# Optimization experiments

Hardware: AMD Instinct MI355X
Metric: run time of the kernel (lower is better)

The kernel has to match this reference:

```python
import jax, jax.numpy as jnp
import numpy as np

S, B, N, K, D, H = 4, 8, 2048, 16, 32, 128


def setup_inputs() -> dict:
    key = jax.random.key(0)
    ks = jax.random.split(key, 7)
    x = jax.random.normal(ks[0], (S, B, N, D), dtype=jnp.float32)
    mu = jax.random.normal(ks[1], (S, B, K, D), dtype=jnp.float32)
    tau = jax.random.uniform(ks[2], (S, B, K, D), dtype=jnp.float32)  # precisions > 0
    # Linear(3D -> H); stored as (3D, H) i.e. transpose of torch's (H, 3D) weight
    W1 = jax.random.normal(ks[3], (3 * D, H), dtype=jnp.float32) * (1.0 / np.sqrt(3 * D))
    b1 = jax.random.normal(ks[4], (H,), dtype=jnp.float32) * 0.01
    W2 = jax.random.normal(ks[5], (H, 1), dtype=jnp.float32) * (1.0 / np.sqrt(H))
    b2 = jax.random.normal(ks[6], (1,), dtype=jnp.float32) * 0.01
    return {"x": x, "mu": mu, "tau": tau, "W1": W1, "b1": b1, "W2": W2, "b2": b2}


def reference(x, mu, tau, W1, b1, W2, b2):
    # Original torch code materializes var = cat([x_expand, mu_expand, tau_expand], -1)
    # of shape (S,B,N,K,3D) then applies Linear(3D,H). Mathematically identical:
    # split W1 rows into the x / mu / tau blocks and add the partial projections,
    # which avoids building the (S,B,N,K,3D) concat tensor.
    d = x.shape[-1]
    Wx, Wm, Wt = W1[:d], W1[d:2 * d], W1[2 * d:]
    hx = jnp.einsum('sbnd,dh->sbnh', x, Wx)                       # (S,B,N,H)
    hk = jnp.einsum('sbkd,dh->sbkh', mu, Wm) \
       + jnp.einsum('sbkd,dh->sbkh', tau, Wt)                     # (S,B,K,H)
    h = jnp.tanh(hx[:, :, :, None, :] + hk[:, :, None, :, :] + b1)  # (S,B,N,K,H)
    gamma = jnp.einsum('sbnkh,h->sbnk', h, W2[:, 0]) + b2[0]        # (S,B,N,K)
    q_probs = jax.nn.softmax(gamma, axis=-1)
    return q_probs
```

## Files before the change

kernel.cpp:

```cpp
#include <hip/hip_runtime.h>
#include <math.h>

typedef _Float16 half_t;
typedef __attribute__((ext_vector_type(8))) _Float16 half8;

#define EXP2F(x) __builtin_amdgcn_exp2f(x)
#define RCPF(x)  __builtin_amdgcn_rcpf(x)
#define C_SCALE 2.8853900817779268f

__global__ __launch_bounds__(256, 4) void fused_kernel(
    const float* __restrict__ x, const float* __restrict__ mu,
    const float* __restrict__ tau, const float* __restrict__ W1,
    const float* __restrict__ b1, const float* __restrict__ W2,
    float* __restrict__ out) {
  __shared__ __align__(16) float  sX[64][36];
  __shared__ __align__(16) half_t sEx[64][136];
  __shared__ __align__(16) half_t sEk[16][136];
  __shared__ __align__(16) half_t sW2[128];

  int t = threadIdx.x;
  int row0 = blockIdx.x * 64;
  int sb = row0 >> 11;

  const float4* x4 = (const float4*)(x + (size_t)row0 * 32);
#pragma unroll
  for (int i = 0; i < 2; ++i) {
    int j = i * 256 + t;
    int n = j >> 3, d4 = j & 7;
    float4 v = x4[j];
    v.x *= C_SCALE; v.y *= C_SCALE; v.z *= C_SCALE; v.w *= C_SCALE;
    *(float4*)&sX[n][d4 * 4] = v;
  }
  if (t < 16) {
    float4 a = ((const float4*)W2)[2 * t];
    float4 b = ((const float4*)W2)[2 * t + 1];
    half8 hv;
    hv[0] = (half_t)(-2.f * a.x); hv[1] = (half_t)(-2.f * a.y);
    hv[2] = (half_t)(-2.f * a.z); hv[3] = (half_t)(-2.f * a.w);
    hv[4] = (half_t)(-2.f * b.x); hv[5] = (half_t)(-2.f * b.y);
    hv[6] = (half_t)(-2.f * b.z); hv[7] = (half_t)(-2.f * b.w);
    *(half8*)&sW2[t * 8] = hv;
  }
  __syncthreads();

  {
    int hg = t & 15, rg = t >> 4;
    int h0 = hg * 8, r0 = rg * 4;
    float acc[4][8];
#pragma unroll
    for (int j = 0; j < 4; ++j)
#pragma unroll
      for (int l = 0; l < 8; ++l) acc[j][l] = 0.f;
    const float* Wp = W1 + h0;
#pragma unroll 4
    for (int d = 0; d < 32; ++d) {
      float4 wa = *(const float4*)(Wp + d * 128);
      float4 wb = *(const float4*)(Wp + d * 128 + 4);
      float w[8] = {wa.x, wa.y, wa.z, wa.w, wb.x, wb.y, wb.z, wb.w};
#pragma unroll
      for (int j = 0; j < 4; ++j) {
        float xv = sX[r0 + j][d];
#pragma unroll
        for (int l = 0; l < 8; ++l) acc[j][l] = fmaf(xv, w[l], acc[j][l]);
      }
    }
#pragma unroll
    for (int j = 0; j < 4; ++j) {
      half8 hv;
#pragma unroll
      for (int l = 0; l < 8; ++l) hv[l] = (half_t)EXP2F(acc[j][l]);
      *(half8*)&sEx[r0 + j][h0] = hv;
    }
  }

  {
    int k = t >> 4, h0 = (t & 15) * 8;
    const float4* mu4  = (const float4*)(mu  + ((size_t)sb * 16 + k) * 32);
    const float4* tau4 = (const float4*)(tau + ((size_t)sb * 16 + k) * 32);
    float acc[8];
    {
      float4 ba = *(const float4*)(b1 + h0);
      float4 bb = *(const float4*)(b1 + h0 + 4);
      acc[0] = ba.x; acc[1] = ba.y; acc[2] = ba.z; acc[3] = ba.w;
      acc[4] = bb.x; acc[5] = bb.y; acc[6] = bb.z; acc[7] = bb.w;
    }
    const float* Wm = W1 + 32 * 128 + h0;
    const float* Wt = W1 + 64 * 128 + h0;
#pragma unroll 2
    for (int d4 = 0; d4 < 8; ++d4) {
      float4 m4 = mu4[d4], t4 = tau4[d4];
      float mv4[4] = {m4.x, m4.y, m4.z, m4.w};
      float tv4[4] = {t4.x, t4.y, t4.z, t4.w};
#pragma unroll
      for (int dd = 0; dd < 4; ++dd) {
        int d = d4 * 4 + dd;
        float4 wma = *(const float4*)(Wm + d * 128);
        float4 wmb = *(const float4*)(Wm + d * 128 + 4);
        float4 wta = *(const float4*)(Wt + d * 128);
        float4 wtb = *(const float4*)(Wt + d * 128 + 4);
        float wm[8] = {wma.x, wma.y, wma.z, wma.w, wmb.x, wmb.y, wmb.z, wmb.w};
        float wt[8] = {wta.x, wta.y, wta.z, wta.w, wtb.x, wtb.y, wtb.z, wtb.w};
        float mv = mv4[dd], tv = tv4[dd];
#pragma unroll
        for (int l = 0; l < 8; ++l) {
          acc[l] = fmaf(mv, wm[l], acc[l]);
          acc[l] = fmaf(tv, wt[l], acc[l]);
        }
      }
    }
    half8 hv;
#pragma unroll
    for (int l = 0; l < 8; ++l) hv[l] = (half_t)EXP2F(C_SCALE * acc[l]);
    *(half8*)&sEk[k][h0] = hv;
  }
  __syncthreads();

  int kg = t & 7, rg = t >> 3;
  int r0 = rg * 2, k0 = kg * 2;
  float a00 = 0.f, a01 = 0.f, a10 = 0.f, a11 = 0.f;
#pragma unroll 2
  for (int h8 = 0; h8 < 16; ++h8) {
    half8 ex0 = *(const half8*)&sEx[r0][h8 * 8];
    half8 ex1 = *(const half8*)&sEx[r0 + 1][h8 * 8];
    half8 ekv0 = *(const half8*)&sEk[k0][h8 * 8];
    half8 ekv1 = *(const half8*)&sEk[k0 + 1][h8 * 8];
    half8 wv = *(const half8*)&sW2[h8 * 8];
#pragma unroll
    for (int j = 0; j < 8; ++j) {
      float e0 = (float)ex0[j], e1 = (float)ex1[j];
      float f0 = (float)ekv0[j], f1 = (float)ekv1[j];
      float w = (float)wv[j];
      a00 = fmaf(w, RCPF(fmaf(e0, f0, 1.0f)), a00);
      a01 = fmaf(w, RCPF(fmaf(e0, f1, 1.0f)), a01);
      a10 = fmaf(w, RCPF(fmaf(e1, f0, 1.0f)), a10);
      a11 = fmaf(w, RCPF(fmaf(e1, f1, 1.0f)), a11);
    }
  }

  const float l2e = 1.4426950408889634f;
  {
    float m = fmaxf(a00, a01);
#pragma unroll
    for (int s = 1; s < 8; s <<= 1) m = fmaxf(m, __shfl_xor(m, s, 8));
    float p0 = EXP2F((a00 - m) * l2e), p1 = EXP2F((a01 - m) * l2e);
    float sum = p0 + p1;
#pragma unroll
    for (int s = 1; s < 8; s <<= 1) sum += __shfl_xor(sum, s, 8);
    float inv = RCPF(sum);
    float2 o = make_float2(p0 * inv, p1 * inv);
    *(float2*)&out[(size_t)(row0 + r0) * 16 + k0] = o;
  }
  {
    float m = fmaxf(a10, a11);
#pragma unroll
    for (int s = 1; s < 8; s <<= 1) m = fmaxf(m, __shfl_xor(m, s, 8));
    float p0 = EXP2F((a10 - m) * l2e), p1 = EXP2F((a11 - m) * l2e);
    float sum = p0 + p1;
#pragma unroll
    for (int s = 1; s < 8; s <<= 1) sum += __shfl_xor(sum, s, 8);
    float inv = RCPF(sum);
    float2 o = make_float2(p0 * inv, p1 * inv);
    *(float2*)&out[(size_t)(row0 + r0 + 1) * 16 + k0] = o;
  }
}

extern "C" void kernel_launch(void* const* d_in, const int* in_sizes, int n_in,
                              void* d_out, int out_size, void* d_ws, size_t ws_size,
                              hipStream_t stream) {
  const float* x   = (const float*)d_in[0];
  const float* mu  = (const float*)d_in[1];
  const float* tau = (const float*)d_in[2];
  const float* W1  = (const float*)d_in[3];
  const float* b1  = (const float*)d_in[4];
  const float* W2  = (const float*)d_in[5];
  float* out = (float*)d_out;
  (void)in_sizes; (void)n_in; (void)out_size; (void)d_ws; (void)ws_size;

  fused_kernel<<<1024, 256, 0, stream>>>(x, mu, tau, W1, b1, W2, out);
}
```

Before: 103.9 us.

## Stage W1 x-block in padded LDS, alias it for Ex, keep Ek/W2 fp32

The x-projection weights (first 32 rows of W1) are now loaded cooperatively into a padded shared buffer, so the per-row projection reads shared memory instead of issuing repeated global float4 loads. That buffer is then reused, after an extra barrier, to hold the fp16 exp(x) tile, and the x projection moves after the mu/tau projection. The Ek and W2 tiles are kept in fp32 rather than fp16, which removes conversions in the inner loop but doubles their LDS reads. The cost is an extra __syncthreads and higher register pressure, since the exp(x) values are held in registers across a barrier.

```diff
diff --git a/kernel.cpp b/kernel.cpp
--- a/kernel.cpp
+++ b/kernel.cpp
@@ -13,10 +13,10 @@
     const float* __restrict__ tau, const float* __restrict__ W1,
     const float* __restrict__ b1, const float* __restrict__ W2,
     float* __restrict__ out) {
-  __shared__ __align__(16) float  sX[64][36];
-  __shared__ __align__(16) half_t sEx[64][136];
-  __shared__ __align__(16) half_t sEk[16][136];
-  __shared__ __align__(16) half_t sW2[128];
+  __shared__ __align__(16) float sX[64][36];
+  __shared__ __align__(16) unsigned char sU[32 * 560];
+  __shared__ __align__(16) float sEk[16][132];
+  __shared__ __align__(16) float sW2[128];
 
   int t = threadIdx.x;
   int row0 = blockIdx.x * 64;
@@ -31,47 +31,13 @@
     v.x *= C_SCALE; v.y *= C_SCALE; v.z *= C_SCALE; v.w *= C_SCALE;
     *(float4*)&sX[n][d4 * 4] = v;
   }
-  if (t < 16) {
-    float4 a = ((const float4*)W2)[2 * t];
-    float4 b = ((const float4*)W2)[2 * t + 1];
-    half8 hv;
-    hv[0] = (half_t)(-2.f * a.x); hv[1] = (half_t)(-2.f * a.y);
-    hv[2] = (half_t)(-2.f * a.z); hv[3] = (half_t)(-2.f * a.w);
-    hv[4] = (half_t)(-2.f * b.x); hv[5] = (half_t)(-2.f * b.y);
-    hv[6] = (half_t)(-2.f * b.z); hv[7] = (half_t)(-2.f * b.w);
-    *(half8*)&sW2[t * 8] = hv;
+#pragma unroll
+  for (int i = 0; i < 4; ++i) {
+    int j = i * 256 + t;
+    int d = j >> 5, f = j & 31;
+    *(float4*)(sU + d * 560 + f * 16 + (f >> 3) * 16) = ((const float4*)W1)[j];
   }
-  __syncthreads();
-
-  {
-    int hg = t & 15, rg = t >> 4;
-    int h0 = hg * 8, r0 = rg * 4;
-    float acc[4][8];
-#pragma unroll
-    for (int j = 0; j < 4; ++j)
-#pragma unroll
-      for (int l = 0; l < 8; ++l) acc[j][l] = 0.f;
-    const float* Wp = W1 + h0;
-#pragma unroll 4
-    for (int d = 0; d < 32; ++d) {
-      float4 wa = *(const float4*)(Wp + d * 128);
-      float4 wb = *(const float4*)(Wp + d * 128 + 4);
-      float w[8] = {wa.x, wa.y, wa.z, wa.w, wb.x, wb.y, wb.z, wb.w};
-#pragma unroll
-      for (int j = 0; j < 4; ++j) {
-        float xv = sX[r0 + j][d];
-#pragma unroll
-        for (int l = 0; l < 8; ++l) acc[j][l] = fmaf(xv, w[l], acc[j][l]);
-      }
-    }
-#pragma unroll
-    for (int j = 0; j < 4; ++j) {
-      half8 hv;
-#pragma unroll
-      for (int l = 0; l < 8; ++l) hv[l] = (half_t)EXP2F(acc[j][l]);
-      *(half8*)&sEx[r0 + j][h0] = hv;
-    }
-  }
+  if (t < 128) sW2[t] = -2.0f * W2[t];
 
   {
     int k = t >> 4, h0 = (t & 15) * 8;
@@ -108,32 +74,74 @@
         }
       }
     }
-    half8 hv;
-#pragma unroll
-    for (int l = 0; l < 8; ++l) hv[l] = (half_t)EXP2F(C_SCALE * acc[l]);
-    *(half8*)&sEk[k][h0] = hv;
+    float4 e0, e1;
+    e0.x = EXP2F(C_SCALE * acc[0]); e0.y = EXP2F(C_SCALE * acc[1]);
+    e0.z = EXP2F(C_SCALE * acc[2]); e0.w = EXP2F(C_SCALE * acc[3]);
+    e1.x = EXP2F(C_SCALE * acc[4]); e1.y = EXP2F(C_SCALE * acc[5]);
+    e1.z = EXP2F(C_SCALE * acc[6]); e1.w = EXP2F(C_SCALE * acc[7]);
+    *(float4*)&sEk[k][h0] = e0;
+    *(float4*)&sEk[k][h0 + 4] = e1;
   }
   __syncthreads();
 
-  int kg = t & 7, rg = t >> 3;
-  int r0 = rg * 2, k0 = kg * 2;
+  int hg = t & 15, rg = t >> 4;
+  int h0 = hg * 8, r0 = rg * 4;
+  half8 hv[4];
+  {
+    const unsigned char* wbase = sU + hg * 32 + (hg >> 2) * 16;
+    float acc[4][8];
+#pragma unroll
+    for (int j = 0; j < 4; ++j)
+#pragma unroll
+      for (int l = 0; l < 8; ++l) acc[j][l] = 0.f;
+#pragma unroll 4
+    for (int d = 0; d < 32; ++d) {
+      float4 wa = *(const float4*)(wbase + d * 560);
+      float4 wb = *(const float4*)(wbase + d * 560 + 16);
+      float w[8] = {wa.x, wa.y, wa.z, wa.w, wb.x, wb.y, wb.z, wb.w};
+#pragma unroll
+      for (int j = 0; j < 4; ++j) {
+        float xv = sX[r0 + j][d];
+#pragma unroll
+        for (int l = 0; l < 8; ++l) acc[j][l] = fmaf(xv, w[l], acc[j][l]);
+      }
+    }
+#pragma unroll
+    for (int j = 0; j < 4; ++j)
+#pragma unroll
+      for (int l = 0; l < 8; ++l) hv[j][l] = (half_t)EXP2F(acc[j][l]);
+  }
+  __syncthreads();
+
+  half_t (*sEx)[136] = (half_t(*)[136])sU;
+#pragma unroll
+  for (int j = 0; j < 4; ++j) *(half8*)&sEx[r0 + j][h0] = hv[j];
+  __syncthreads();
+
+  int kg = t & 7, rg2 = t >> 3;
+  int rp = rg2 * 2, k0 = kg * 2;
   float a00 = 0.f, a01 = 0.f, a10 = 0.f, a11 = 0.f;
 #pragma unroll 2
   for (int h8 = 0; h8 < 16; ++h8) {
-    half8 ex0 = *(const half8*)&sEx[r0][h8 * 8];
-    half8 ex1 = *(const half8*)&sEx[r0 + 1][h8 * 8];
-    half8 ekv0 = *(const half8*)&sEk[k0][h8 * 8];
-    half8 ekv1 = *(const half8*)&sEk[k0 + 1][h8 * 8];
-    half8 wv = *(const half8*)&sW2[h8 * 8];
+    half8 ex0 = *(const half8*)&sEx[rp][h8 * 8];
+    half8 ex1 = *(const half8*)&sEx[rp + 1][h8 * 8];
+    float4 f0a = *(const float4*)&sEk[k0][h8 * 8];
+    float4 f0b = *(const float4*)&sEk[k0][h8 * 8 + 4];
+    float4 f1a = *(const float4*)&sEk[k0 + 1][h8 * 8];
+    float4 f1b = *(const float4*)&sEk[k0 + 1][h8 * 8 + 4];
+    float4 wva = *(const float4*)&sW2[h8 * 8];
+    float4 wvb = *(const float4*)&sW2[h8 * 8 + 4];
+    float f0[8] = {f0a.x, f0a.y, f0a.z, f0a.w, f0b.x, f0b.y, f0b.z, f0b.w};
+    float f1[8] = {f1a.x, f1a.y, f1a.z, f1a.w, f1b.x, f1b.y, f1b.z, f1b.w};
+    float wv[8] = {wva.x, wva.y, wva.z, wva.w, wvb.x, wvb.y, wvb.z, wvb.w};
 #pragma unroll
     for (int j = 0; j < 8; ++j) {
       float e0 = (float)ex0[j], e1 = (float)ex1[j];
-      float f0 = (float)ekv0[j], f1 = (float)ekv1[j];
-      float w = (float)wv[j];
-      a00 = fmaf(w, RCPF(fmaf(e0, f0, 1.0f)), a00);
-      a01 = fmaf(w, RCPF(fmaf(e0, f1, 1.0f)), a01);
-      a10 = fmaf(w, RCPF(fmaf(e1, f0, 1.0f)), a10);
-      a11 = fmaf(w, RCPF(fmaf(e1, f1, 1.0f)), a11);
+      float w = wv[j];
+      a00 = fmaf(w, RCPF(fmaf(e0, f0[j], 1.0f)), a00);
+      a01 = fmaf(w, RCPF(fmaf(e0, f1[j], 1.0f)), a01);
+      a10 = fmaf(w, RCPF(fmaf(e1, f0[j], 1.0f)), a10);
+      a11 = fmaf(w, RCPF(fmaf(e1, f1[j], 1.0f)), a11);
     }
   }
 
@@ -148,7 +156,7 @@
     for (int s = 1; s < 8; s <<= 1) sum += __shfl_xor(sum, s, 8);
     float inv = RCPF(sum);
     float2 o = make_float2(p0 * inv, p1 * inv);
-    *(float2*)&out[(size_t)(row0 + r0) * 16 + k0] = o;
+    *(float2*)&out[(size_t)(row0 + rp) * 16 + k0] = o;
   }
   {
     float m = fmaxf(a10, a11);
@@ -160,7 +168,7 @@
     for (int s = 1; s < 8; s <<= 1) sum += __shfl_xor(sum, s, 8);
     float inv = RCPF(sum);
     float2 o = make_float2(p0 * inv, p1 * inv);
-    *(float2*)&out[(size_t)(row0 + r0 + 1) * 16 + k0] = o;
+    *(float2*)&out[(size_t)(row0 + rp + 1) * 16 + k0] = o;
   }
 }
 
```

Measured after the change: 98.68 us. 1.05x faster.

## Stage Wx in LDS, double block size, and alias sEx onto the weight buffer

Applied to the files above, without the earlier changes.

Each block now processes 128 rows with 512 threads, and the first 32 rows of W1 (Wx) are staged into a padded LDS buffer instead of being read from global memory inside the x-projection loop. That buffer is reused as sEx after an extra barrier, and the mu/tau projection is spread over 512 threads. The aim is to cut repeated global or L2 reads of W1 and to halve per-block setup across fewer, larger blocks. In exchange there are extra __syncthreads, more LDS per block, and only 512 blocks, which may lower occupancy.

```diff
diff --git a/kernel.cpp b/kernel.cpp
--- a/kernel.cpp
+++ b/kernel.cpp
@@ -3,33 +3,40 @@
 
 typedef _Float16 half_t;
 typedef __attribute__((ext_vector_type(8))) _Float16 half8;
+typedef __attribute__((ext_vector_type(4))) _Float16 half4;
 
 #define EXP2F(x) __builtin_amdgcn_exp2f(x)
 #define RCPF(x)  __builtin_amdgcn_rcpf(x)
 #define C_SCALE 2.8853900817779268f
 
-__global__ __launch_bounds__(256, 4) void fused_kernel(
+__global__ __launch_bounds__(512, 4) void fused_kernel(
     const float* __restrict__ x, const float* __restrict__ mu,
     const float* __restrict__ tau, const float* __restrict__ W1,
     const float* __restrict__ b1, const float* __restrict__ W2,
     float* __restrict__ out) {
-  __shared__ __align__(16) float  sX[64][36];
-  __shared__ __align__(16) half_t sEx[64][136];
+  __shared__ __align__(16) float sX[128][36];
+  __shared__ __align__(16) unsigned char sU[128 * 272];
   __shared__ __align__(16) half_t sEk[16][136];
   __shared__ __align__(16) half_t sW2[128];
 
   int t = threadIdx.x;
-  int row0 = blockIdx.x * 64;
+  int row0 = blockIdx.x * 128;
   int sb = row0 >> 11;
 
   const float4* x4 = (const float4*)(x + (size_t)row0 * 32);
 #pragma unroll
   for (int i = 0; i < 2; ++i) {
-    int j = i * 256 + t;
+    int j = i * 512 + t;
     int n = j >> 3, d4 = j & 7;
     float4 v = x4[j];
     v.x *= C_SCALE; v.y *= C_SCALE; v.z *= C_SCALE; v.w *= C_SCALE;
     *(float4*)&sX[n][d4 * 4] = v;
+  }
+#pragma unroll
+  for (int i = 0; i < 2; ++i) {
+    int j = i * 512 + t;
+    int d = j >> 5, f = j & 31;
+    *(float4*)(sU + d * 560 + f * 16 + (f >> 3) * 16) = ((const float4*)W1)[j];
   }
   if (t < 16) {
     float4 a = ((const float4*)W2)[2 * t];
@@ -41,48 +48,15 @@
     hv[6] = (half_t)(-2.f * b.z); hv[7] = (half_t)(-2.f * b.w);
     *(half8*)&sW2[t * 8] = hv;
   }
-  __syncthreads();
 
   {
-    int hg = t & 15, rg = t >> 4;
-    int h0 = hg * 8, r0 = rg * 4;
-    float acc[4][8];
-#pragma unroll
-    for (int j = 0; j < 4; ++j)
-#pragma unroll
-      for (int l = 0; l < 8; ++l) acc[j][l] = 0.f;
-    const float* Wp = W1 + h0;
-#pragma unroll 4
-    for (int d = 0; d < 32; ++d) {
-      float4 wa = *(const float4*)(Wp + d * 128);
-      float4 wb = *(const float4*)(Wp + d * 128 + 4);
-      float w[8] = {wa.x, wa.y, wa.z, wa.w, wb.x, wb.y, wb.z, wb.w};
-#pragma unroll
-      for (int j = 0; j < 4; ++j) {
-        float xv = sX[r0 + j][d];
-#pragma unroll
-        for (int l = 0; l < 8; ++l) acc[j][l] = fmaf(xv, w[l], acc[j][l]);
-      }
-    }
-#pragma unroll
-    for (int j = 0; j < 4; ++j) {
-      half8 hv;
-#pragma unroll
-      for (int l = 0; l < 8; ++l) hv[l] = (half_t)EXP2F(acc[j][l]);
-      *(half8*)&sEx[r0 + j][h0] = hv;
-    }
-  }
-
-  {
-    int k = t >> 4, h0 = (t & 15) * 8;
+    int k = t >> 5, h0 = (t & 31) * 4;
     const float4* mu4  = (const float4*)(mu  + ((size_t)sb * 16 + k) * 32);
     const float4* tau4 = (const float4*)(tau + ((size_t)sb * 16 + k) * 32);
-    float acc[8];
+    float acc[4];
     {
       float4 ba = *(const float4*)(b1 + h0);
-      float4 bb = *(const float4*)(b1 + h0 + 4);
       acc[0] = ba.x; acc[1] = ba.y; acc[2] = ba.z; acc[3] = ba.w;
-      acc[4] = bb.x; acc[5] = bb.y; acc[6] = bb.z; acc[7] = bb.w;
     }
     const float* Wm = W1 + 32 * 128 + h0;
     const float* Wt = W1 + 64 * 128 + h0;
@@ -94,42 +68,78 @@
 #pragma unroll
       for (int dd = 0; dd < 4; ++dd) {
         int d = d4 * 4 + dd;
-        float4 wma = *(const float4*)(Wm + d * 128);
-        float4 wmb = *(const float4*)(Wm + d * 128 + 4);
-        float4 wta = *(const float4*)(Wt + d * 128);
-        float4 wtb = *(const float4*)(Wt + d * 128 + 4);
-        float wm[8] = {wma.x, wma.y, wma.z, wma.w, wmb.x, wmb.y, wmb.z, wmb.w};
-        float wt[8] = {wta.x, wta.y, wta.z, wta.w, wtb.x, wtb.y, wtb.z, wtb.w};
+        float4 wm = *(const float4*)(Wm + d * 128);
+        float4 wt = *(const float4*)(Wt + d * 128);
+        float wmv[4] = {wm.x, wm.y, wm.z, wm.w};
+        float wtv[4] = {wt.x, wt.y, wt.z, wt.w};
         float mv = mv4[dd], tv = tv4[dd];
 #pragma unroll
-        for (int l = 0; l < 8; ++l) {
-          acc[l] = fmaf(mv, wm[l], acc[l]);
-          acc[l] = fmaf(tv, wt[l], acc[l]);
+        for (int l = 0; l < 4; ++l) {
+          acc[l] = fmaf(mv, wmv[l], acc[l]);
+          acc[l] = fmaf(tv, wtv[l], acc[l]);
         }
       }
     }
-    half8 hv;
+    half4 hv;
 #pragma unroll
-    for (int l = 0; l < 8; ++l) hv[l] = (half_t)EXP2F(C_SCALE * acc[l]);
-    *(half8*)&sEk[k][h0] = hv;
+    for (int l = 0; l < 4; ++l) hv[l] = (half_t)EXP2F(C_SCALE * acc[l]);
+    *(half4*)&sEk[k][h0] = hv;
   }
   __syncthreads();
 
-  int kg = t & 7, rg = t >> 3;
-  int r0 = rg * 2, k0 = kg * 2;
+  int hg = t & 15, rg = t >> 4;
+  int h0 = hg * 8, r0 = rg * 4;
+  half8 hv[4];
+  {
+    const unsigned char* wbase = sU + hg * 32 + (hg >> 2) * 16;
+    float acc[4][8];
+#pragma unroll
+    for (int j = 0; j < 4; ++j)
+#pragma unroll
+      for (int l = 0; l < 8; ++l) acc[j][l] = 0.f;
+#pragma unroll 4
+    for (int d = 0; d < 32; ++d) {
+      float4 wa = *(const float4*)(wbase + d * 560);
+      float4 wb = *(const float4*)(wbase + d * 560 + 16);
+      float w[8] = {wa.x, wa.y, wa.z, wa.w, wb.x, wb.y, wb.z, wb.w};
+#pragma unroll
+      for (int j = 0; j < 4; ++j) {
+        float xv = sX[r0 + j][d];
+#pragma unroll
+        for (int l = 0; l < 8; ++l) acc[j][l] = fmaf(xv, w[l], acc[j][l]);
+      }
+    }
+#pragma unroll
+    for (int j = 0; j < 4; ++j)
+#pragma unroll
+      for (int l = 0; l < 8; ++l) hv[j][l] = (half_t)EXP2F(acc[j][l]);
+  }
+  __syncthreads();
+
+  half_t (*sEx)[136] = (half_t(*)[136])sU;
+#pragma unroll
+  for (int j = 0; j < 4; ++j) *(half8*)&sEx[r0 + j][h0] = hv[j];
+  __syncthreads();
+
+  int kg = t & 7, rg2 = t >> 3;
+  int rp = rg2 * 2, k0 = kg * 2;
+  const half_t* exr0 = &sEx[rp][0];
+  const half_t* exr1 = &sEx[rp + 1][0];
+  const half_t* ekr0 = &sEk[k0][0];
+  const half_t* ekr1 = &sEk[k0 + 1][0];
   float a00 = 0.f, a01 = 0.f, a10 = 0.f, a11 = 0.f;
-#pragma unroll 2
+#pragma unroll
   for (int h8 = 0; h8 < 16; ++h8) {
-    half8 ex0 = *(const half8*)&sEx[r0][h8 * 8];
-    half8 ex1 = *(const half8*)&sEx[r0 + 1][h8 * 8];
-    half8 ekv0 = *(const half8*)&sEk[k0][h8 * 8];
-    half8 ekv1 = *(const half8*)&sEk[k0 + 1][h8 * 8];
-    half8 wv = *(const half8*)&sW2[h8 * 8];
+    half8 ex0  = *(const half8*)(exr0 + h8 * 8);
+    half8 ex1  = *(const half8*)(exr1 + h8 * 8);
+    half8 ekv0 = *(const half8*)(ekr0 + h8 * 8);
+    half8 ekv1 = *(const half8*)(ekr1 + h8 * 8);
+    half8 wv   = *(const half8*)(&sW2[h8 * 8]);
 #pragma unroll
     for (int j = 0; j < 8; ++j) {
       float e0 = (float)ex0[j], e1 = (float)ex1[j];
       float f0 = (float)ekv0[j], f1 = (float)ekv1[j];
-      float w = (float)wv[j];
+      float w  = (float)wv[j];
       a00 = fmaf(w, RCPF(fmaf(e0, f0, 1.0f)), a00);
       a01 = fmaf(w, RCPF(fmaf(e0, f1, 1.0f)), a01);
       a10 = fmaf(w, RCPF(fmaf(e1, f0, 1.0f)), a10);
@@ -148,7 +158,7 @@
     for (int s = 1; s < 8; s <<= 1) sum += __shfl_xor(sum, s, 8);
     float inv = RCPF(sum);
     float2 o = make_float2(p0 * inv, p1 * inv);
-    *(float2*)&out[(size_t)(row0 + r0) * 16 + k0] = o;
+    *(float2*)&out[(size_t)(row0 + rp) * 16 + k0] = o;
   }
   {
     float m = fmaxf(a10, a11);
@@ -160,7 +170,7 @@
     for (int s = 1; s < 8; s <<= 1) sum += __shfl_xor(sum, s, 8);
     float inv = RCPF(sum);
     float2 o = make_float2(p0 * inv, p1 * inv);
-    *(float2*)&out[(size_t)(row0 + r0 + 1) * 16 + k0] = o;
+    *(float2*)&out[(size_t)(row0 + rp + 1) * 16 + k0] = o;
   }
 }
 
@@ -176,5 +186,5 @@
   float* out = (float*)d_out;
   (void)in_sizes; (void)n_in; (void)out_size; (void)d_ws; (void)ws_size;
 
-  fused_kernel<<<1024, 256, 0, stream>>>(x, mu, tau, W1, b1, W2, out);
+  fused_kernel<<<512, 512, 0, stream>>>(x, mu, tau, W1, b1, W2, out);
 }
```

Result: faster. 97.68 us (-5.9%).
